# Optimization experiments

Measured on AMD Instinct MI355X. Metric: run time of the kernel, lower is better.

## Reference

```python
import jax, jax.numpy as jnp
import numpy as np
from jax import lax

DN = ('NCHW', 'OIHW', 'NCHW')


def conv2d(x, w, b, pad):
    y = lax.conv_general_dilated(x, w, (1, 1), [(pad, pad), (pad, pad)], dimension_numbers=DN)
    return y + b[None, :, None, None]


def unfold3x3(x):
    # x: [B, C, H, W] -> [B, C, 9, H, W], matching F.unfold(kernel=3, padding=1)
    B, C, H, W = x.shape
    xp = jnp.pad(x, ((0, 0), (0, 0), (1, 1), (1, 1)))
    views = [xp[:, :, ki:ki + H, kj:kj + W] for ki in range(3) for kj in range(3)]
    return jnp.stack(views, axis=2)


def setup_inputs() -> dict:
    key = jax.random.key(0)
    ks = jax.random.split(key, 4)
    B, C, H, W = 16, 1, 512, 512
    hid, up_h, up_w = 32, 1, 3
    x = jax.random.normal(ks[0], (B, C, H, W), dtype=jnp.float32)
    w1 = jax.random.normal(ks[1], (hid, C, 3, 3), dtype=jnp.float32) * (1.0 / 3.0)
    b1 = jnp.zeros((hid,), dtype=jnp.float32)
    alpha = jnp.full((hid,), 0.25, dtype=jnp.float32)  # PReLU init
    w2 = jax.random.normal(ks[2], (9 * up_h * up_w, hid, 1, 1), dtype=jnp.float32) * (1.0 / np.sqrt(hid))
    b2 = jnp.zeros((9 * up_h * up_w,), dtype=jnp.float32)
    return {"x": x, "target_h": H * up_h, "target_w": W * up_w,
            "w1": w1, "b1": b1, "alpha": alpha, "w2": w2, "b2": b2}


def reference(x, target_h, target_w, w1, b1, alpha, w2, b2):
    B, C, H, W = x.shape
    up_h = target_h // H  # = 1
    up_w = target_w // W  # = 3
    # mask_net: conv3x3 -> PReLU -> conv1x1
    h = conv2d(x, w1, b1, pad=1)
    h = jnp.where(h > 0, h, alpha[None, :, None, None] * h)
    mask = conv2d(h, w2, b2, pad=0)  # [B, 9*up_h*up_w, H, W]
    # convex upsample (anisotropic)
    neigh = unfold3x3(x)  # [B, C, 9, H, W]
    m = mask.reshape(B, 9, up_h, up_w, H, W)
    m = jax.nn.softmax(m, axis=1)
    up = jnp.einsum('bckhw,bkuvhw->bcuvhw', neigh, m)  # [B,C,up_h,up_w,H,W]
    up = up.transpose(0, 1, 4, 2, 5, 3)  # [B,C,H,up_h,W,up_w]
    return up.reshape(B, C, H * up_h, W * up_w)
```

## Files before the change

### kernel.cpp

```cpp
#include <hip/hip_runtime.h>
#include <hip/hip_bf16.h>


#define BB 16
#define HH 512
#define WW 512
#define HID 32
#define NM 27
#define LOG2E 1.44269504088896340736f
#define NT 16384
#define NBLK 1280
#define ROWB 112
#define ZOFF (64 * ROWB)

typedef short bf16x8 __attribute__((ext_vector_type(8)));
typedef float f32x4  __attribute__((ext_vector_type(4)));
typedef unsigned int u32;
typedef u32 u32x4 __attribute__((ext_vector_type(4)));

__device__ __forceinline__ u32 pk2(float a, float b) {
    union { __hip_bfloat162 h2; u32 u; } cv;
    cv.h2 = __float22bfloat162_rn(make_float2(a, b));
    return cv.u;
}

__device__ __forceinline__ void lds_fence() {
    asm volatile("" ::: "memory");
    __builtin_amdgcn_sched_barrier(0);
}

__device__ __forceinline__ void load_xv(const float* __restrict__ x, int tile,
                                        int tid, float xv[9]) {
    const int p    = tile * 256 + tid;
    const int wcol = p & (WW - 1);
    const int t    = p >> 9;
    const int hrow = t & (HH - 1);
    const int bidx = t >> 9;
    const float* xb = x + (size_t)bidx * (HH * WW);
    int hy[3], wx[3];
    bool hok[3], wok[3];
#pragma unroll
    for (int i = 0; i < 3; ++i) {
        const int h = hrow + i - 1;
        hok[i] = (unsigned)h < (unsigned)HH;
        hy[i]  = h < 0 ? 0 : (h > HH - 1 ? HH - 1 : h);
        const int w = wcol + i - 1;
        wok[i] = (unsigned)w < (unsigned)WW;
        wx[i]  = w < 0 ? 0 : (w > WW - 1 ? WW - 1 : w);
    }
#pragma unroll
    for (int ki = 0; ki < 3; ++ki)
#pragma unroll
        for (int kj = 0; kj < 3; ++kj) {
            const float v = xb[hy[ki] * WW + wx[kj]];
            xv[ki * 3 + kj] = (hok[ki] && wok[kj]) ? v : 0.0f;
        }
}

__global__ void prep_B(const float* __restrict__ w1, const float* __restrict__ b1,
                       const float* __restrict__ alpha, const float* __restrict__ w2,
                       const float* __restrict__ b2, __hip_bfloat16* __restrict__ ws) {
    const int i = blockIdx.x * 256 + threadIdx.x;
    if (i >= 3072) return;
    const int sec = i >> 10;
    const int r   = i & 1023;
    const int n   = r >> 5, k = r & 31;
    float v = 0.0f;
    if (sec == 0) {
        if (n < NM) {
            if (k < 9) {
                for (int c = 0; c < HID; ++c)
                    v += w2[n * HID + c] * (0.5f * (1.0f + alpha[c])) * w1[c * 9 + k];
            } else if (k == 9) {
                v = b2[n];
                for (int c = 0; c < HID; ++c)
                    v += w2[n * HID + c] * (0.5f * (1.0f + alpha[c])) * b1[c];
            }
        }
        v *= LOG2E;
    } else if (sec == 1) {
        if (n < NM) {
            const int c = ((k & 4) ? 16 : 0) + (k >> 3) * 4 + (k & 3);
            v = w2[n * HID + c] * (0.5f * (1.0f - alpha[c])) * LOG2E;
        }
    } else {
        v = (k < 9) ? w1[n * 9 + k] : (k == 9 ? b1[n] : 0.0f);
    }
    ws[i] = __float2bfloat16(v);
}

__global__ __launch_bounds__(256, 5) void convex_upsample_mfma9(
    const float* __restrict__ x,
    const __hip_bfloat16* __restrict__ ws,
    float* __restrict__ out)
{
    __shared__ char lds_raw[4][ZOFF + 16];

    const int tid  = threadIdx.x;
    const int wv   = tid >> 6;
    const int lane = tid & 63;
    const int l16  = lane & 15;
    const int lq   = lane >> 4;
    char* wbase = lds_raw[wv];

    bf16x8 Bf2[2], M2p[2], Bf1[2];
#pragma unroll
    for (int nt = 0; nt < 2; ++nt) {
        const int ro = (nt * 16 + l16) * 32 + lq * 8;
        Bf2[nt] = *(const bf16x8*)(ws + ro);
        M2p[nt] = *(const bf16x8*)(ws + 1024 + ro);
        Bf1[nt] = *(const bf16x8*)(ws + 2048 + ro);
    }

    *(u32x4*)(wbase + ZOFF) = (u32x4){0u, 0u, 0u, 0u};

    int tb = blockIdx.x;
    float xv[9];
    load_xv(x, tb, tid, xv);

    while (tb < NT) {
        const int tn  = tb + NBLK;
        const int tpf = (tn < NT) ? tn : 0;
        float xn[9];
        load_xv(x, tpf, tid, xn);

        char* myrow = wbase + lane * ROWB;
        *(u32x4*)(myrow)      = (u32x4){pk2(xv[0], xv[1]), pk2(xv[2], xv[3]),
                                        pk2(xv[4], xv[5]), pk2(xv[6], xv[7])};
        *(u32x4*)(myrow + 16) = (u32x4){pk2(xv[8], 1.0f), 0u, 0u, 0u};

        lds_fence();

        bf16x8 a0[4];
#pragma unroll
        for (int mt = 0; mt < 4; ++mt) {
            const char* ab = wbase + (mt * 16 + l16) * ROWB;
            const char* aptr = (lq < 2) ? (ab + lq * 16) : (wbase + ZOFF);
            a0[mt] = *(const bf16x8*)aptr;
        }

        lds_fence();

#pragma unroll
        for (int mt = 0; mt < 4; ++mt) {
            char* ab = wbase + (mt * 16 + l16) * ROWB;
            f32x4 z0 = {0.f, 0.f, 0.f, 0.f}, z1 = {0.f, 0.f, 0.f, 0.f};
            z0 = __builtin_amdgcn_mfma_f32_16x16x32_bf16(Bf1[0], a0[mt], z0, 0, 0, 0);
            z1 = __builtin_amdgcn_mfma_f32_16x16x32_bf16(Bf1[1], a0[mt], z1, 0, 0, 0);
            union { u32 u[4]; bf16x8 h; } zf;
            zf.u[0] = pk2(fabsf(z0[0]), fabsf(z0[1]));
            zf.u[1] = pk2(fabsf(z0[2]), fabsf(z0[3]));
            zf.u[2] = pk2(fabsf(z1[0]), fabsf(z1[1]));
            zf.u[3] = pk2(fabsf(z1[2]), fabsf(z1[3]));
            f32x4 c0 = {0.f, 0.f, 0.f, 0.f}, c1 = {0.f, 0.f, 0.f, 0.f};
            c0 = __builtin_amdgcn_mfma_f32_16x16x32_bf16(M2p[0], zf.h,   c0, 0, 0, 0);
            c0 = __builtin_amdgcn_mfma_f32_16x16x32_bf16(Bf2[0], a0[mt], c0, 0, 0, 0);
            c1 = __builtin_amdgcn_mfma_f32_16x16x32_bf16(M2p[1], zf.h,   c1, 0, 0, 0);
            c1 = __builtin_amdgcn_mfma_f32_16x16x32_bf16(Bf2[1], a0[mt], c1, 0, 0, 0);
            *(f32x4*)(ab + 48 + lq * 16) = c0;
            if (lq < 3) *(f32x4*)(ab + lq * 16) = c1;
        }

        lds_fence();

        f32x4 mv[7];
#pragma unroll
        for (int q = 0; q < 4; ++q)
            mv[q] = *(const f32x4*)(myrow + 48 + q * 16);
#pragma unroll
        for (int q = 0; q < 3; ++q)
            mv[4 + q] = *(const f32x4*)(myrow + q * 16);

        const int p    = tb * 256 + tid;
        const int wcol = p & (WW - 1);
        const int t    = p >> 9;
        const int hrow = t & (HH - 1);
        const int bidx = t >> 9;
        const size_t ob = ((size_t)(bidx * HH + hrow) * (WW * 3)) + (size_t)wcol * 3;
#pragma unroll
        for (int v = 0; v < 3; ++v) {
            float ssum = 0.0f, acc = 0.0f;
#pragma unroll
            for (int k = 0; k < 9; ++k) {
                const int j = k * 3 + v;
                const float lg = (j < 16) ? mv[j >> 2][j & 3]
                                          : mv[4 + ((j - 16) >> 2)][(j - 16) & 3];
                const float e = __builtin_amdgcn_exp2f(lg);
                ssum += e;
                acc = fmaf(xv[k], e, acc);
            }
            out[ob + v] = acc * __builtin_amdgcn_rcpf(ssum);
        }

        lds_fence();

        tb = tn;
#pragma unroll
        for (int k = 0; k < 9; ++k) xv[k] = xn[k];
    }
}

extern "C" void kernel_launch(void* const* d_in, const int* in_sizes, int n_in,
                              void* d_out, int out_size, void* d_ws, size_t ws_size,
                              hipStream_t stream) {
    const float* x     = (const float*)d_in[0];
    const float* w1    = (const float*)d_in[3];
    const float* b1    = (const float*)d_in[4];
    const float* alpha = (const float*)d_in[5];
    const float* w2    = (const float*)d_in[6];
    const float* b2    = (const float*)d_in[7];
    float* out = (float*)d_out;
    __hip_bfloat16* ws = (__hip_bfloat16*)d_ws;

    hipLaunchKernelGGL(prep_B, dim3(12), dim3(256), 0, stream, w1, b1, alpha, w2, b2, ws);
    hipLaunchKernelGGL(convex_upsample_mfma9, dim3(NBLK), dim3(256), 0, stream,
                       x, ws, out);
}
```

Before: 61.10 us.

## Software-pipeline softmax blend of previous tile behind MFMA of current tile

Restructures the persistent loop so the exp/softmax/weighted-sum and output store for tile i run between the LDS operand loads and the MFMA chain of tile i+1. This lets the transcendental and store work overlap the matrix-core work, with an epilogue after the loop for the last tile. The blend now uses the bf16-packed neighbour values instead of fp32, which lowers precision. Launch bounds drop from 5 to 4 waves to make room for the extra live registers. The first iteration writes a placeholder zero to the first tile, which the next iteration overwrites.

```diff
diff --git a/kernel.cpp b/kernel.cpp
--- a/kernel.cpp
+++ b/kernel.cpp
@@ -55,6 +55,32 @@
             const float v = xb[hy[ki] * WW + wx[kj]];
             xv[ki * 3 + kj] = (hok[ki] && wok[kj]) ? v : 0.0f;
         }
+}
+
+__device__ __forceinline__ void softmax_store(const f32x4 mv[7], const u32 pxp[5],
+                                              int p, float* __restrict__ out) {
+    float xq[9];
+#pragma unroll
+    for (int i = 0; i < 4; ++i) {
+        xq[2 * i]     = __uint_as_float(pxp[i] << 16);
+        xq[2 * i + 1] = __uint_as_float(pxp[i] & 0xffff0000u);
+    }
+    xq[8] = __uint_as_float(pxp[4] << 16);
+    const size_t ob = (size_t)p * 3;
+#pragma unroll
+    for (int v = 0; v < 3; ++v) {
+        float ssum = 0.0f, acc = 0.0f;
+#pragma unroll
+        for (int k = 0; k < 9; ++k) {
+            const int j = k * 3 + v;
+            const float lg = (j < 16) ? mv[j >> 2][j & 3]
+                                      : mv[4 + ((j - 16) >> 2)][(j - 16) & 3];
+            const float e = __builtin_amdgcn_exp2f(lg);
+            ssum += e;
+            acc = fmaf(xq[k], e, acc);
+        }
+        out[ob + v] = acc * __builtin_amdgcn_rcpf(ssum);
+    }
 }
 
 __global__ void prep_B(const float* __restrict__ w1, const float* __restrict__ b1,
@@ -89,7 +115,7 @@
     ws[i] = __float2bfloat16(v);
 }
 
-__global__ __launch_bounds__(256, 5) void convex_upsample_mfma9(
+__global__ __launch_bounds__(256, 4) void convex_upsample_mfma10(
     const float* __restrict__ x,
     const __hip_bfloat16* __restrict__ ws,
     float* __restrict__ out)
@@ -117,6 +143,14 @@
     int tb = blockIdx.x;
     float xv[9];
     load_xv(x, tb, tid, xv);
+    u32 px[5] = {pk2(xv[0], xv[1]), pk2(xv[2], xv[3]), pk2(xv[4], xv[5]),
+                 pk2(xv[6], xv[7]), pk2(xv[8], 1.0f)};
+
+    f32x4 mv[7];
+#pragma unroll
+    for (int q = 0; q < 7; ++q) mv[q] = (f32x4){0.f, 0.f, 0.f, 0.f};
+    u32 pxp[5] = {0u, 0u, 0u, 0u, 0u};
+    int pp = tb * 256 + tid;
 
     while (tb < NT) {
         const int tn  = tb + NBLK;
@@ -125,9 +159,8 @@
         load_xv(x, tpf, tid, xn);
 
         char* myrow = wbase + lane * ROWB;
-        *(u32x4*)(myrow)      = (u32x4){pk2(xv[0], xv[1]), pk2(xv[2], xv[3]),
-                                        pk2(xv[4], xv[5]), pk2(xv[6], xv[7])};
-        *(u32x4*)(myrow + 16) = (u32x4){pk2(xv[8], 1.0f), 0u, 0u, 0u};
+        *(u32x4*)(myrow)      = (u32x4){px[0], px[1], px[2], px[3]};
+        *(u32x4*)(myrow + 16) = (u32x4){px[4], 0u, 0u, 0u};
 
         lds_fence();
 
@@ -140,6 +173,8 @@
         }
 
         lds_fence();
+
+        softmax_store(mv, pxp, pp, out);
 
 #pragma unroll
         for (int mt = 0; mt < 4; ++mt) {
@@ -163,7 +198,6 @@
 
         lds_fence();
 
-        f32x4 mv[7];
 #pragma unroll
         for (int q = 0; q < 4; ++q)
             mv[q] = *(const f32x4*)(myrow + 48 + q * 16);
@@ -171,33 +205,19 @@
         for (int q = 0; q < 3; ++q)
             mv[4 + q] = *(const f32x4*)(myrow + q * 16);
 
-        const int p    = tb * 256 + tid;
-        const int wcol = p & (WW - 1);
-        const int t    = p >> 9;
-        const int hrow = t & (HH - 1);
-        const int bidx = t >> 9;
-        const size_t ob = ((size_t)(bidx * HH + hrow) * (WW * 3)) + (size_t)wcol * 3;
-#pragma unroll
-        for (int v = 0; v < 3; ++v) {
-            float ssum = 0.0f, acc = 0.0f;
-#pragma unroll
-            for (int k = 0; k < 9; ++k) {
-                const int j = k * 3 + v;
-                const float lg = (j < 16) ? mv[j >> 2][j & 3]
-                                          : mv[4 + ((j - 16) >> 2)][(j - 16) & 3];
-                const float e = __builtin_amdgcn_exp2f(lg);
-                ssum += e;
-                acc = fmaf(xv[k], e, acc);
-            }
-            out[ob + v] = acc * __builtin_amdgcn_rcpf(ssum);
-        }
+#pragma unroll
+        for (int i = 0; i < 5; ++i) pxp[i] = px[i];
+        pp = tb * 256 + tid;
+        px[0] = pk2(xn[0], xn[1]); px[1] = pk2(xn[2], xn[3]);
+        px[2] = pk2(xn[4], xn[5]); px[3] = pk2(xn[6], xn[7]);
+        px[4] = pk2(xn[8], 1.0f);
 
         lds_fence();
 
         tb = tn;
-#pragma unroll
-        for (int k = 0; k < 9; ++k) xv[k] = xn[k];
-    }
+    }
+
+    softmax_store(mv, pxp, pp, out);
 }
 
 extern "C" void kernel_launch(void* const* d_in, const int* in_sizes, int n_in,
@@ -213,6 +233,6 @@
     __hip_bfloat16* ws = (__hip_bfloat16*)d_ws;
 
     hipLaunchKernelGGL(prep_B, dim3(12), dim3(256), 0, stream, w1, b1, alpha, w2, b2, ws);
-    hipLaunchKernelGGL(convex_upsample_mfma9, dim3(NBLK), dim3(256), 0, stream,
+    hipLaunchKernelGGL(convex_upsample_mfma10, dim3(NBLK), dim3(256), 0, stream,
                        x, ws, out);
 }
```

Measured after the change: 71.28 us. +16.7%, slower.
